# Optimization experiments

Measured on AMD Instinct MI355X. Metric: run time of the kernel, lower is better.

Reference implementation:

```python
import jax, jax.numpy as jnp
import numpy as np

STRIDES = (8, 16, 32)
NC = 80            # num_classes
BINS = 16          # dfl_bins
TOPK = 10          # tal_topk
TAL_ALPHA, TAL_BETA = 0.5, 6.0   # ultralytics TaskAlignedAssigner defaults
EPS = 1e-9
FOCAL_A, FOCAL_G = 0.25, 2.0
W_CLS, W_IOU, W_DFL = 0.5, 7.5, 1.5


def _make_grid(H, W, stride):
    ys, xs = jnp.meshgrid(jnp.arange(H, dtype=jnp.float32), jnp.arange(W, dtype=jnp.float32), indexing='ij')
    return jnp.stack([(xs + 0.5) * stride, (ys + 0.5) * stride], -1).reshape(H * W, 2)


def _flatten(p):
    # (B,C,H,W) -> cls (B,N,NC), dfl (B,N,4,BINS); channel layout = [4*BINS dfl | NC cls]
    B, C, H, W = p.shape
    p = p.transpose(0, 2, 3, 1).reshape(B, H * W, C)
    return p[..., 4 * BINS:], p[..., :4 * BINS].reshape(B, H * W, 4, BINS)


def _pairwise_iou(gt, pr):
    # gt (B,G,4), pr (B,N,4) -> iou (B,G,N)
    g = gt[:, :, None]
    p = pr[:, None]
    lt = jnp.maximum(g[..., :2], p[..., :2])
    rb = jnp.minimum(g[..., 2:], p[..., 2:])
    wh = jnp.clip(rb - lt, 0.0)
    inter = wh[..., 0] * wh[..., 1]
    ag = (g[..., 2] - g[..., 0]) * (g[..., 3] - g[..., 1])
    ap = jnp.clip(p[..., 2] - p[..., 0], 0.0) * jnp.clip(p[..., 3] - p[..., 1], 0.0)
    return inter / (ag + ap - inter + EPS)


def _ciou_loss(p, t):
    # elementwise CIoU loss, (...,4) xyxy -> (...)
    px1, py1, px2, py2 = p[..., 0], p[..., 1], p[..., 2], p[..., 3]
    tx1, ty1, tx2, ty2 = t[..., 0], t[..., 1], t[..., 2], t[..., 3]
    w1, h1 = px2 - px1, py2 - py1
    w2, h2 = tx2 - tx1, ty2 - ty1
    inter = jnp.clip(jnp.minimum(px2, tx2) - jnp.maximum(px1, tx1), 0.0) * \
            jnp.clip(jnp.minimum(py2, ty2) - jnp.maximum(py1, ty1), 0.0)
    union = w1 * h1 + w2 * h2 - inter + EPS
    iou = inter / union
    cw = jnp.maximum(px2, tx2) - jnp.minimum(px1, tx1)
    ch = jnp.maximum(py2, ty2) - jnp.minimum(py1, ty1)
    c2 = cw * cw + ch * ch + EPS
    rho2 = ((px1 + px2 - tx1 - tx2) ** 2 + (py1 + py2 - ty1 - ty2) ** 2) / 4.0
    v = (4.0 / np.pi ** 2) * (jnp.arctan(w2 / (h2 + EPS)) - jnp.arctan(w1 / (h1 + EPS))) ** 2
    alpha = jax.lax.stop_gradient(v / (v - iou + (1.0 + EPS)))
    return 1.0 - (iou - rho2 / c2 - v * alpha)


def _tal_assign(cls_prob, pred_boxes, grids, gt_bboxes, gt_labels):
    B, N, C = cls_prob.shape
    G = gt_bboxes.shape[1]
    idx = jnp.broadcast_to(gt_labels[:, None, :], (B, N, G))
    scores = jnp.take_along_axis(cls_prob, idx, axis=2).transpose(0, 2, 1)  # (B,G,N)
    overlaps = _pairwise_iou(gt_bboxes, pred_boxes)                          # (B,G,N)
    align = scores ** TAL_ALPHA * overlaps ** TAL_BETA
    x, y = grids[:, 0], grids[:, 1]
    in_gts = ((x[None, None] > gt_bboxes[..., 0:1]) & (x[None, None] < gt_bboxes[..., 2:3]) &
              (y[None, None] > gt_bboxes[..., 1:2]) & (y[None, None] < gt_bboxes[..., 3:4]))
    metric = jnp.where(in_gts, align, 0.0)
    vals, idxs = jax.lax.top_k(metric, TOPK)                                 # (B,G,TOPK)
    bi = jnp.arange(B)[:, None, None]
    gi = jnp.arange(G)[None, :, None]
    topk_mask = jnp.zeros((B, G, N), bool).at[bi, gi, idxs].set(vals > EPS)
    mask_pos = topk_mask & in_gts
    multi = mask_pos.sum(1) > 1                                              # (B,N)
    is_max = jnp.argmax(overlaps, 1)[:, None, :] == jnp.arange(G)[None, :, None]
    mask_pos = jnp.where(multi[:, None, :], is_max, mask_pos)
    fg = mask_pos.any(1)                                                     # (B,N)
    matched = jnp.argmax(mask_pos, 1)                                        # (B,N)
    mi = jnp.where(fg, matched, -1)
    b2 = jnp.arange(B)[:, None]
    tb = gt_bboxes[b2, matched]                                              # (B,N,4)
    tl = gt_labels[b2, matched]                                              # (B,N)
    mpf = mask_pos.astype(align.dtype)
    align_m = align * mpf
    ov_m = overlaps * mpf
    norm = (align_m * ov_m.max(-1, keepdims=True) / (align_m.max(-1, keepdims=True) + EPS)).max(1)
    ts = jax.nn.one_hot(tl, C, dtype=align.dtype) * norm[..., None] * fg[..., None]
    return ts, tb, fg, mi


def _dfl_targets(gt_bboxes, mi, fgf, grids, stride_map):
    # vectorized version of _make_dfl_targets: soft two-bin scatter per coord
    B, N = mi.shape
    b2 = jnp.arange(B)[:, None]
    boxes = gt_bboxes[b2, jnp.maximum(mi, 0)]                                # (B,N,4)
    cx, cy = grids[:, 0], grids[:, 1]
    d = jnp.stack([jnp.clip(cx - boxes[..., 0], 0.0), jnp.clip(cy - boxes[..., 1], 0.0),
                   jnp.clip(boxes[..., 2] - cx, 0.0), jnp.clip(boxes[..., 3] - cy, 0.0)], -1)
    d = jnp.clip(d / stride_map[None, :, None], 0.0, BINS - 1 - 1e-6)
    lo = jnp.floor(d)
    a = d - lo
    lo_i = lo.astype(jnp.int32)
    up_i = jnp.minimum(lo_i + 1, BINS - 1)
    td = jax.nn.one_hot(lo_i, BINS) * (1.0 - a)[..., None] + jax.nn.one_hot(up_i, BINS) * a[..., None]
    return td * fgf[..., None, None]                                         # (B,N,4,BINS)


def _focal_sum(logits, targets):
    logits = logits.reshape(-1, NC)
    targets = targets.reshape(-1, NC)
    p = jax.nn.sigmoid(logits)
    # stable BCE-with-logits
    ce = jnp.maximum(logits, 0.0) - logits * targets + jnp.log1p(jnp.exp(-jnp.abs(logits)))
    p_t = p * targets + (1.0 - p) * (1.0 - targets)
    a_t = targets * FOCAL_A + (1.0 - targets) * (1.0 - FOCAL_A)
    return (a_t * (1.0 - p_t) ** FOCAL_G * ce).sum()


def _loss(p0, p1, p2, gt_bboxes, gt_labels):
    cls_l, dfl_l, grid_l, str_l = [], [], [], []
    for p, s in zip((p0, p1, p2), STRIDES):
        c, d = _flatten(p)
        cls_l.append(c)
        dfl_l.append(d)
        H, W = p.shape[2], p.shape[3]
        grid_l.append(_make_grid(H, W, s))
        str_l.append(jnp.full((H * W,), float(s), jnp.float32))
    all_cls = jnp.concatenate(cls_l, 1)       # (B,N,NC)
    all_dfl = jnp.concatenate(dfl_l, 1)       # (B,N,4,BINS)
    grids = jnp.concatenate(grid_l, 0)        # (N,2)
    stride_map = jnp.concatenate(str_l, 0)    # (N,)
    # DFL decode: expectation over bins * stride -> ltrb -> xyxy
    dist = (jax.nn.softmax(all_dfl, -1) * jnp.arange(BINS, dtype=jnp.float32)).sum(-1) * stride_map[None, :, None]
    cx, cy = grids[:, 0], grids[:, 1]
    pred_boxes = jnp.stack([cx - dist[..., 0], cy - dist[..., 1], cx + dist[..., 2], cy + dist[..., 3]], -1)
    # assignment under stop_gradient (torch.no_grad in the original)
    cls_prob = jax.lax.stop_gradient(jax.nn.sigmoid(all_cls))
    pb_sg = jax.lax.stop_gradient(pred_boxes)
    ts, tb, fg, mi = _tal_assign(cls_prob, pb_sg, grids, gt_bboxes, gt_labels)
    ts = jax.lax.stop_gradient(ts)
    tb = jax.lax.stop_gradient(tb)
    fgf = fg.astype(jnp.float32)
    den = jnp.maximum(fg.sum(), 1).astype(jnp.float32)
    loss_iou = (_ciou_loss(pred_boxes, tb) * fgf).sum() / den
    tdfl = _dfl_targets(gt_bboxes, mi, fgf, grids, stride_map)
    loss_dfl = -(tdfl * jax.nn.log_softmax(all_dfl, -1)).sum() / den
    loss_cls = _focal_sum(all_cls, ts) / den
    return jnp.stack([W_IOU * loss_iou, W_DFL * loss_dfl, W_CLS * loss_cls])


def setup_inputs() -> dict:
    key = jax.random.key(0)
    ks = jax.random.split(key, 5)
    B, G = 16, 32
    p0 = jax.random.normal(ks[0], (B, 4 * BINS + NC, 80, 80), jnp.float32)
    p1 = jax.random.normal(ks[1], (B, 4 * BINS + NC, 40, 40), jnp.float32)
    p2 = jax.random.normal(ks[2], (B, 4 * BINS + NC, 20, 20), jnp.float32)
    u = jax.random.uniform(ks[3], (B, G, 4), jnp.float32)
    x1 = u[..., 0] * 560.0
    y1 = u[..., 1] * 560.0
    w = u[..., 2] * 140.0 + 20.0
    h = u[..., 3] * 140.0 + 20.0
    gt_bboxes = jnp.stack([x1, y1, jnp.minimum(x1 + w, 640.0), jnp.minimum(y1 + h, 640.0)], -1)
    gt_labels = jax.random.randint(ks[4], (B, G), 0, NC, jnp.int32)
    return {"p0": p0, "p1": p1, "p2": p2, "gt_bboxes": gt_bboxes, "gt_labels": gt_labels}


def reference(p0, p1, p2, gt_bboxes, gt_labels):
    return _loss(p0, p1, p2, gt_bboxes, gt_labels)
```

## Files before the change

kernel.cpp:

```cpp
#include <hip/hip_runtime.h>
#include <hip/hip_bf16.h>
#include <math.h>

#define NCC 80
#define BINS 16
#define NCH 144
#define NB 16
#define NG 32
#define NA 8400
#define HW0 6400
#define HW1 1600
#define HW2 400
#define TOPKK 10
#define EPSF 1e-9f
#define MAXC 832
#define MAXFG (NB*NG*TOPKK)
#define FGB2 20
#define NMASK (NB*NA)
#define DEC_BLOCKS 525
#define FOCAL_BLOCKS 2625
#define MAIN_BLOCKS (DEC_BLOCKS + FOCAL_BLOCKS)

__device__ __forceinline__ void anchor_geom(int n, float& cx, float& cy, float& st){
    if(n < HW0){ int y=n/80, x=n-y*80; st=8.f; cx=(x+0.5f)*8.f; cy=(y+0.5f)*8.f; }
    else if(n < HW0+HW1){ int m=n-HW0; int y=m/40, x=m-y*40; st=16.f; cx=(x+0.5f)*16.f; cy=(y+0.5f)*16.f; }
    else { int m=n-(HW0+HW1); int y=m/20, x=m-y*20; st=32.f; cx=(x+0.5f)*32.f; cy=(y+0.5f)*32.f; }
}

__device__ __forceinline__ const float* level_base(const float* p0, const float* p1, const float* p2,
                                                   int b, int n, int& m, int& hw){
    if(n < HW0){ m=n; hw=HW0; return p0 + (size_t)b*NCH*HW0; }
    if(n < HW0+HW1){ m=n-HW0; hw=HW1; return p1 + (size_t)b*NCH*HW1; }
    m=n-(HW0+HW1); hw=HW2; return p2 + (size_t)b*NCH*HW2;
}

__device__ __forceinline__ float iou_gp(float gx1,float gy1,float gx2,float gy2,
                                        float px1,float py1,float px2,float py2){
    float ltx = fmaxf(gx1, px1), lty = fmaxf(gy1, py1);
    float rbx = fminf(gx2, px2), rby = fminf(gy2, py2);
    float w = fmaxf(rbx-ltx, 0.f), h = fmaxf(rby-lty, 0.f);
    float inter = w*h;
    float ag = (gx2-gx1)*(gy2-gy1);
    float ap = fmaxf(px2-px1,0.f)*fmaxf(py2-py1,0.f);
    return inter/(ag+ap-inter+EPSF);
}

__device__ __forceinline__ float focal0(float x, float& p, float& ce0){
    float ax = fabsf(x);
    float e  = __expf(-ax);
    float r  = 1.f/(1.f+e);
    p   = (x >= 0.f) ? r : 1.f - r;
    ce0 = fmaxf(x,0.f) + __logf(1.f+e);
    return 0.75f*p*p*ce0;
}

__global__ __launch_bounds__(256) void k_main(const float* __restrict__ p0, const float* __restrict__ p1,
                                              const float* __restrict__ p2, float* __restrict__ boxc,
                                              float* __restrict__ lsev,
                                              unsigned* __restrict__ maskg, float* __restrict__ amax,
                                              float* __restrict__ omax, int* __restrict__ cnt,
                                              float* __restrict__ pcls){
    int tid = threadIdx.x;
    if(blockIdx.x < DEC_BLOCKS){
        int l = blockIdx.x*256 + tid;
        maskg[l] = 0u;
        if(l < NB*NG){ amax[l] = 0.f; omax[l] = 0.f; }
        if(l == 0) *cnt = 0;
        int q = l % 2100;
        int j = (l / 2100) & 3;
        int b = l / 8400;
        const float* pl; int hw, m, n0, D; float st;
        if(q < 1600){ pl=p0; hw=HW0; m=4*q;        n0=m;         D=80; st=8.f; }
        else if(q < 2000){ pl=p1; hw=HW1; m=4*(q-1600); n0=HW0+m;     D=40; st=16.f; }
        else { pl=p2; hw=HW2; m=4*(q-2000); n0=HW0+HW1+m; D=20; st=32.f; }
        const float* ch = pl + ((size_t)b*NCH + j*BINS)*hw + m;
        float4 v[BINS];
        float4 mx = make_float4(-1e30f,-1e30f,-1e30f,-1e30f);
        #pragma unroll
        for(int k=0;k<BINS;k++){
            v[k] = *(const float4*)(ch + (size_t)k*hw);
            mx.x=fmaxf(mx.x,v[k].x); mx.y=fmaxf(mx.y,v[k].y);
            mx.z=fmaxf(mx.z,v[k].z); mx.w=fmaxf(mx.w,v[k].w);
        }
        float4 s = make_float4(0,0,0,0), acc = make_float4(0,0,0,0);
        #pragma unroll
        for(int k=0;k<BINS;k++){
            float fk=(float)k; float e;
            e=__expf(v[k].x-mx.x); s.x+=e; acc.x+=e*fk;
            e=__expf(v[k].y-mx.y); s.y+=e; acc.y+=e*fk;
            e=__expf(v[k].z-mx.z); s.z+=e; acc.z+=e*fk;
            e=__expf(v[k].w-mx.w); s.w+=e; acc.w+=e*fk;
        }
        float4 lse = make_float4(mx.x+__logf(s.x), mx.y+__logf(s.y),
                                 mx.z+__logf(s.z), mx.w+__logf(s.w));
        *(float4*)(lsev + (size_t)j*NB*NA + (size_t)b*NA + n0) = lse;
        float4 d = make_float4(acc.x/s.x*st, acc.y/s.y*st, acc.z/s.z*st, acc.w/s.w*st);
        int row = m / D, col = m - row*D;
        float cy = (row+0.5f)*st;
        float cx0=(col+0.5f)*st, cx1=(col+1.5f)*st, cx2=(col+2.5f)*st, cx3=(col+3.5f)*st;
        float4 o;
        if(j==0)      o = make_float4(cx0-d.x, cx1-d.y, cx2-d.z, cx3-d.w);
        else if(j==1) o = make_float4(cy -d.x, cy -d.y, cy -d.z, cy -d.w);
        else if(j==2) o = make_float4(cx0+d.x, cx1+d.y, cx2+d.z, cx3+d.w);
        else          o = make_float4(cy +d.x, cy +d.y, cy +d.z, cy +d.w);
        *(float4*)(boxc + (size_t)j*NB*NA + (size_t)b*NA + n0) = o;
    } else {
        __shared__ float s4[4];
        int blk = blockIdx.x - DEC_BLOCKS;
        int t = blk*256 + tid;
        float acc = 0.f;
        #pragma unroll
        for(int it=0; it<4; ++it){
            int i4 = t + it*672000;
            const float4* src;
            if(i4 < 2048000){
                int b = i4 / 128000; int r = i4 - b*128000;
                src = (const float4*)(p0 + (size_t)b*921600 + 409600) + r;
            } else if(i4 < 2560000){
                int j = i4 - 2048000; int b = j / 32000; int r = j - b*32000;
                src = (const float4*)(p1 + (size_t)b*230400 + 102400) + r;
            } else {
                int j = i4 - 2560000; int b = j / 8000; int r = j - b*8000;
                src = (const float4*)(p2 + (size_t)b*57600 + 25600) + r;
            }
            float4 x4 = *src;
            float p, c;
            acc += focal0(x4.x, p, c);
            acc += focal0(x4.y, p, c);
            acc += focal0(x4.z, p, c);
            acc += focal0(x4.w, p, c);
        }
        #pragma unroll
        for(int off=32; off; off>>=1) acc += __shfl_down(acc, off);
        if((tid&63)==0) s4[tid>>6] = acc;
        __syncthreads();
        if(tid==0) pcls[blk] = s4[0]+s4[1]+s4[2]+s4[3];
    }
}

__global__ __launch_bounds__(256) void k_assign(const float* __restrict__ p0, const float* __restrict__ p1,
                                                const float* __restrict__ p2, const float* __restrict__ boxc,
                                                const float* __restrict__ gtb, const int* __restrict__ gtl,
                                                unsigned* __restrict__ maskg){
    __shared__ float metric[MAXC];
    __shared__ int   candn[MAXC];
    __shared__ float rv[4]; __shared__ int ri[4];
    __shared__ float sbest;
    int g = blockIdx.x, b = blockIdx.y, tid = threadIdx.x;
    const float* gb = gtb + ((size_t)b*NG + g)*4;
    float gx1=gb[0], gy1=gb[1], gx2=gb[2], gy2=gb[3];
    int label = gtl[b*NG+g];
    const float* bx1 = boxc + (size_t)b*NA;
    const float* by1 = bx1 + (size_t)NB*NA;
    const float* bx2 = by1 + (size_t)NB*NA;
    const float* by2 = bx2 + (size_t)NB*NA;

    int xs[3], ys[3], nxv[3], cc[3];
    #pragma unroll
    for(int lvl=0; lvl<3; lvl++){
        float s = (float)(8<<lvl); int D = 80>>lvl;
        int x0 = max(0, (int)floorf(gx1/s - 0.5f));
        int x1 = min(D-1, (int)ceilf (gx2/s - 0.5f));
        int y0 = max(0, (int)floorf(gy1/s - 0.5f));
        int y1 = min(D-1, (int)ceilf (gy2/s - 0.5f));
        xs[lvl]=x0; ys[lvl]=y0;
        nxv[lvl]=max(0, x1-x0+1);
        int nyv=max(0, y1-y0+1);
        cc[lvl]=nxv[lvl]*nyv;
    }
    int t0 = cc[0], t01 = cc[0]+cc[1], total = t01+cc[2];

    for(int c=tid; c<total; c+=256){
        int lvl, rel;
        if(c < t0){ lvl=0; rel=c; }
        else if(c < t01){ lvl=1; rel=c-t0; }
        else { lvl=2; rel=c-t01; }
        int yy = ys[lvl] + rel / nxv[lvl];
        int xx = xs[lvl] + rel % nxv[lvl];
        int D = 80>>lvl; float s = (float)(8<<lvl);
        int off = (lvl==0)?0:((lvl==1)?HW0:(HW0+HW1));
        int n = off + yy*D + xx;
        float cx = (xx+0.5f)*s, cy = (yy+0.5f)*s;
        float met = 0.f;
        if((cx>gx1)&&(cx<gx2)&&(cy>gy1)&&(cy<gy2)){
            float ov = iou_gp(gx1,gy1,gx2,gy2, bx1[n],by1[n],bx2[n],by2[n]);
            int m,hw; const float* base = level_base(p0,p1,p2,b,n,m,hw);
            float x = base[(size_t)(4*BINS+label)*hw + m];
            float sg = 1.f/(1.f+__expf(-x));
            float o2 = ov*ov;
            met = sqrtf(sg)*(o2*o2*o2);
        }
        metric[c] = met; candn[c] = n;
    }
    __syncthreads();

    for(int k=0;k<TOPKK;k++){
        float bv = -1.f; int bi = 0x7fffffff;
        for(int c=tid; c<total; c+=256){
            float v = metric[c];
            if(v > bv){ bv=v; bi=c; }
        }
        #pragma unroll
        for(int o=1; o<64; o<<=1){
            float ov = __shfl_xor(bv, o);
            int   oi = __shfl_xor(bi, o);
            if(ov > bv || (ov == bv && oi < bi)){ bv=ov; bi=oi; }
        }
        if((tid&63)==0){ rv[tid>>6]=bv; ri[tid>>6]=bi; }
        __syncthreads();
        if(tid==0){
            float fb=rv[0]; int fi=ri[0];
            #pragma unroll
            for(int w=1; w<4; w++)
                if(rv[w]>fb || (rv[w]==fb && ri[w]<fi)){ fb=rv[w]; fi=ri[w]; }
            sbest = fb;
            if(fb > EPSF){
                metric[fi] = -1.f;
                atomicOr(&maskg[(size_t)b*NA + candn[fi]], 1u<<g);
            }
        }
        __syncthreads();
        if(sbest <= EPSF) break;
    }
}

__global__ __launch_bounds__(256) void k_resolve(const float* __restrict__ p0, const float* __restrict__ p1,
                                                 const float* __restrict__ p2, const float* __restrict__ boxc,
                                                 const float* __restrict__ gtb, const int* __restrict__ gtl,
                                                 const unsigned* __restrict__ maskg,
                                                 float* __restrict__ amax, float* __restrict__ omax,
                                                 int* __restrict__ cnt, unsigned* __restrict__ fglist,
                                                 float* __restrict__ fgalign, float* __restrict__ fgx){
    __shared__ float sgt[NG*4];
    __shared__ int wcnt[4];
    __shared__ int sbase;
    int tid = threadIdx.x; int b = blockIdx.y;
    int wv = tid >> 6, lane = tid & 63;
    if(tid < NG*4) sgt[tid] = gtb[(size_t)b*NG*4 + tid];
    __syncthreads();
    int n = blockIdx.x*256 + tid;
    size_t bn = (size_t)b*NA + n;
    unsigned mask = (n < NA) ? maskg[bn] : 0u;
    bool fg = (mask != 0u);

    int match = 0; float ov = 0.f, av = 0.f, x = 0.f;
    if(fg){
        float px1 = boxc[bn], py1 = boxc[(size_t)NB*NA+bn],
              px2 = boxc[2*(size_t)NB*NA+bn], py2 = boxc[3*(size_t)NB*NA+bn];
        if(__popc(mask) > 1){
            float best = -1.f; int bi = 0;
            for(int g=0; g<NG; g++){
                float o = iou_gp(sgt[g*4],sgt[g*4+1],sgt[g*4+2],sgt[g*4+3],px1,py1,px2,py2);
                if(o > best){ best=o; bi=g; }
            }
            match = bi; ov = best;
        } else {
            match = __ffs(mask)-1;
            ov = iou_gp(sgt[match*4],sgt[match*4+1],sgt[match*4+2],sgt[match*4+3],px1,py1,px2,py2);
        }
        int label = gtl[b*NG+match];
        int m,hw; const float* base = level_base(p0,p1,p2,b,n,m,hw);
        x = base[(size_t)(4*BINS+label)*hw + m];
        float sg = 1.f/(1.f+__expf(-x));
        float ov2 = ov*ov;
        av = sqrtf(sg)*(ov2*ov2*ov2);
        atomicMax((int*)&amax[b*NG+match], __float_as_int(av));
        atomicMax((int*)&omax[b*NG+match], __float_as_int(ov));
    }
    unsigned long long bal = __ballot(fg);
    if(lane==0) wcnt[wv] = __popcll(bal);
    __syncthreads();
    if(tid==0){
        int tot = wcnt[0]+wcnt[1]+wcnt[2]+wcnt[3];
        sbase = tot ? atomicAdd(cnt, tot) : 0;
    }
    __syncthreads();
    if(fg){
        int woff = 0;
        for(int w=0; w<wv; w++) woff += wcnt[w];
        int before = __popcll(bal & ((1ull<<lane)-1ull));
        int pos = sbase + woff + before;
        fglist[pos]  = (unsigned)bn | ((unsigned)match << 18);
        fgalign[pos] = av;
        fgx[pos]     = x;
    }
}

__global__ __launch_bounds__(256) void k_fg(const float* __restrict__ p0, const float* __restrict__ p1,
                                            const float* __restrict__ p2, const float* __restrict__ boxc,
                                            const float* __restrict__ lsev, const float* __restrict__ gtb,
                                            const float* __restrict__ amax, const float* __restrict__ omax,
                                            const int* __restrict__ cnt, const unsigned* __restrict__ fglist,
                                            const float* __restrict__ fgalign, const float* __restrict__ fgx,
                                            float* __restrict__ piou, float* __restrict__ pdfl,
                                            float* __restrict__ pfix){
    __shared__ float siou[4], sdfl[4], sfix[4];
    int tid = threadIdx.x, wv = tid>>6, lane = tid&63;
    int i = blockIdx.x*256 + tid;
    float iou_l = 0.f, dfl_l = 0.f, fix_l = 0.f;
    if(i < *cnt){
        unsigned e = fglist[i];
        int bn = e & 0x3FFFF;
        int g  = e >> 18;
        int b  = bn / NA;
        int n  = bn - b*NA;
        float align = fgalign[i];
        float norm = align * omax[b*NG+g] / (amax[b*NG+g] + EPSF);
        const float* gb = gtb + ((size_t)b*NG+g)*4;
        float tx1=gb[0], ty1=gb[1], tx2=gb[2], ty2=gb[3];
        float px1 = boxc[bn], py1 = boxc[(size_t)NB*NA+bn],
              px2 = boxc[2*(size_t)NB*NA+bn], py2 = boxc[3*(size_t)NB*NA+bn];
        int m,hw; const float* base = level_base(p0,p1,p2,b,n,m,hw);
        float cx,cy,st; anchor_geom(n,cx,cy,st);
        float dt4[4] = { cx-tx1, cy-ty1, tx2-cx, ty2-cy };
        #pragma unroll
        for(int j=0;j<4;j++){
            float d = fminf(fmaxf(dt4[j],0.f)/st, 14.999999f);
            float lo = floorf(d); float a = d-lo;
            int li = (int)lo; int ui = min(li+1, BINS-1);
            float lse = lsev[(size_t)j*NB*NA + bn];
            float xlo = base[(size_t)(j*BINS+li)*hw + m];
            float xup = base[(size_t)(j*BINS+ui)*hw + m];
            dfl_l += -((1.f-a)*(xlo-lse) + a*(xup-lse));
        }
        float w1=px2-px1, h1=py2-py1, w2=tx2-tx1, h2=ty2-ty1;
        float inter = fmaxf(fminf(px2,tx2)-fmaxf(px1,tx1),0.f) *
                      fmaxf(fminf(py2,ty2)-fmaxf(py1,ty1),0.f);
        float uni = w1*h1 + w2*h2 - inter + EPSF;
        float iou = inter/uni;
        float cwd = fmaxf(px2,tx2)-fminf(px1,tx1);
        float chd = fmaxf(py2,ty2)-fminf(py1,ty1);
        float c2 = cwd*cwd + chd*chd + EPSF;
        float dx = px1+px2-tx1-tx2, dy = py1+py2-ty1-ty2;
        float rho2 = (dx*dx + dy*dy)*0.25f;
        float dv = atanf(w2/(h2+EPSF)) - atanf(w1/(h1+EPSF));
        float v = 0.40528473456935108577f*dv*dv;
        float alpha = v/(v - iou + 1.f + EPSF);
        iou_l = 1.f - (iou - rho2/c2 - v*alpha);
        float fx = fgx[i];
        float p, ce0;
        float f0 = focal0(fx, p, ce0);
        float tv = norm;
        float cet = ce0 - fx*tv;
        float pt = p*tv + (1.f-p)*(1.f-tv);
        float at = 0.25f*tv + 0.75f*(1.f-tv);
        float om = 1.f-pt;
        fix_l = at*om*om*cet - f0;
    }
    #pragma unroll
    for(int o=32; o; o>>=1){
        iou_l += __shfl_down(iou_l, o);
        dfl_l += __shfl_down(dfl_l, o);
        fix_l += __shfl_down(fix_l, o);
    }
    if(lane==0){ siou[wv]=iou_l; sdfl[wv]=dfl_l; sfix[wv]=fix_l; }
    __syncthreads();
    if(tid==0){
        piou[blockIdx.x] = siou[0]+siou[1]+siou[2]+siou[3];
        pdfl[blockIdx.x] = sdfl[0]+sdfl[1]+sdfl[2]+sdfl[3];
        pfix[blockIdx.x] = sfix[0]+sfix[1]+sfix[2]+sfix[3];
    }
}

__global__ __launch_bounds__(256) void k_final(const float* __restrict__ pcls, const float* __restrict__ piou,
                                               const float* __restrict__ pdfl, const float* __restrict__ pfix,
                                               const int* __restrict__ cnt, float* __restrict__ out){
    __shared__ float sa[4], sb[4], sc[4], sd[4];
    int tid = threadIdx.x, wv = tid>>6, lane = tid&63;
    float A = 0.f, B = 0.f, C = 0.f, D = 0.f;
    for(int t=tid; t<FOCAL_BLOCKS; t+=256) A += pcls[t];
    if(tid < FGB2){ B = piou[tid]; C = pdfl[tid]; D = pfix[tid]; }
    #pragma unroll
    for(int o=32; o; o>>=1){
        A += __shfl_down(A, o);
        B += __shfl_down(B, o);
        C += __shfl_down(C, o);
        D += __shfl_down(D, o);
    }
    if(lane==0){ sa[wv]=A; sb[wv]=B; sc[wv]=C; sd[wv]=D; }
    __syncthreads();
    if(tid==0){
        float a  = sa[0]+sa[1]+sa[2]+sa[3];
        float bb = sb[0]+sb[1]+sb[2]+sb[3];
        float cc = sc[0]+sc[1]+sc[2]+sc[3];
        float dd = sd[0]+sd[1]+sd[2]+sd[3];
        int c = *cnt;
        float den = (float)(c > 1 ? c : 1);
        out[0] = 7.5f * bb / den;
        out[1] = 1.5f * cc / den;
        out[2] = 0.5f * (a + dd) / den;
    }
}

extern "C" void kernel_launch(void* const* d_in, const int* in_sizes, int n_in,
                              void* d_out, int out_size, void* d_ws, size_t ws_size,
                              hipStream_t stream) {
    (void)in_sizes; (void)n_in; (void)out_size; (void)ws_size;
    const float* p0  = (const float*)d_in[0];
    const float* p1  = (const float*)d_in[1];
    const float* p2  = (const float*)d_in[2];
    const float* gtb = (const float*)d_in[3];
    const int*   gtl = (const int*)d_in[4];
    float* out = (float*)d_out;

    char* ws = (char*)d_ws;
    const size_t COMP = (size_t)NB*NA*4;
    size_t off = 0;
    int*      cnt    = (int*)     (ws + off); off += 16;
    float*    amax   = (float*)   (ws + off); off += NB*NG*4;
    float*    omax   = (float*)   (ws + off); off += NB*NG*4;
    unsigned* maskg  = (unsigned*)(ws + off); off += COMP;
    float*    boxc   = (float*)   (ws + off); off += 4*COMP;
    float*    lsev   = (float*)   (ws + off); off += 4*COMP;
    unsigned* fglist = (unsigned*)(ws + off); off += MAXFG*4;
    float*    fgalign= (float*)   (ws + off); off += MAXFG*4;
    float*    fgx    = (float*)   (ws + off); off += MAXFG*4;
    float*    pcls   = (float*)   (ws + off); off += FOCAL_BLOCKS*4;
    float*    piou   = (float*)   (ws + off); off += FGB2*4;
    float*    pdfl   = (float*)   (ws + off); off += FGB2*4;
    float*    pfix   = (float*)   (ws + off); off += FGB2*4;

    dim3 blk(256);
    k_main   <<<MAIN_BLOCKS,   blk, 0, stream>>>(p0,p1,p2, boxc, lsev, maskg, amax, omax, cnt, pcls);
    k_assign <<<dim3(NG,NB),   blk, 0, stream>>>(p0,p1,p2, boxc, gtb, gtl, maskg);
    k_resolve<<<dim3(33,NB),   blk, 0, stream>>>(p0,p1,p2, boxc, gtb, gtl, maskg,
                                                 amax, omax, cnt, fglist, fgalign, fgx);
    k_fg     <<<FGB2,          blk, 0, stream>>>(p0,p1,p2, boxc, lsev, gtb, amax, omax,
                                                 cnt, fglist, fgalign, fgx, piou, pdfl, pfix);
    k_final  <<<1,             blk, 0, stream>>>(pcls, piou, pdfl, pfix, cnt, out);
}
```

Before: 144.6 us.

## Fuse foreground CIoU/DFL loss into resolve kernel and focal fix into final

Removes the separate k_fg launch. The CIoU and DFL terms, which need no global normalization, are now computed directly in k_resolve, with per-block partial sums written out. The focal correction depends on the global amax/omax, so it moves into the single-block k_final, which loops over all foreground entries. This saves one kernel launch and the compacted-list round trip, at the cost of serializing the focal-fix work (up to about 5k entries) in one block and adding divergent work in the resolve blocks.

```diff
diff --git a/kernel.cpp b/kernel.cpp
--- a/kernel.cpp
+++ b/kernel.cpp
@@ -15,8 +15,8 @@
 #define EPSF 1e-9f
 #define MAXC 832
 #define MAXFG (NB*NG*TOPKK)
-#define FGB2 20
 #define NMASK (NB*NA)
+#define NRES 528
 #define DEC_BLOCKS 525
 #define FOCAL_BLOCKS 2625
 #define MAIN_BLOCKS (DEC_BLOCKS + FOCAL_BLOCKS)
@@ -226,14 +226,17 @@
 
 __global__ __launch_bounds__(256) void k_resolve(const float* __restrict__ p0, const float* __restrict__ p1,
                                                  const float* __restrict__ p2, const float* __restrict__ boxc,
+                                                 const float* __restrict__ lsev,
                                                  const float* __restrict__ gtb, const int* __restrict__ gtl,
                                                  const unsigned* __restrict__ maskg,
                                                  float* __restrict__ amax, float* __restrict__ omax,
-                                                 int* __restrict__ cnt, unsigned* __restrict__ fglist,
-                                                 float* __restrict__ fgalign, float* __restrict__ fgx){
+                                                 int* __restrict__ cnt, int* __restrict__ fgbg,
+                                                 float* __restrict__ fgalign, float* __restrict__ fgx,
+                                                 float* __restrict__ piou, float* __restrict__ pdfl){
     __shared__ float sgt[NG*4];
     __shared__ int wcnt[4];
     __shared__ int sbase;
+    __shared__ float siou[4], sdfl[4];
     int tid = threadIdx.x; int b = blockIdx.y;
     int wv = tid >> 6, lane = tid & 63;
     if(tid < NG*4) sgt[tid] = gtb[(size_t)b*NG*4 + tid];
@@ -243,10 +246,12 @@
     unsigned mask = (n < NA) ? maskg[bn] : 0u;
     bool fg = (mask != 0u);
 
-    int match = 0; float ov = 0.f, av = 0.f, x = 0.f;
+    int match = 0; float av = 0.f, x = 0.f;
+    float iou_l = 0.f, dfl_l = 0.f;
     if(fg){
         float px1 = boxc[bn], py1 = boxc[(size_t)NB*NA+bn],
               px2 = boxc[2*(size_t)NB*NA+bn], py2 = boxc[3*(size_t)NB*NA+bn];
+        float ov;
         if(__popc(mask) > 1){
             float best = -1.f; int bi = 0;
             for(int g=0; g<NG; g++){
@@ -266,51 +271,21 @@
         av = sqrtf(sg)*(ov2*ov2*ov2);
         atomicMax((int*)&amax[b*NG+match], __float_as_int(av));
         atomicMax((int*)&omax[b*NG+match], __float_as_int(ov));
-    }
-    unsigned long long bal = __ballot(fg);
-    if(lane==0) wcnt[wv] = __popcll(bal);
-    __syncthreads();
-    if(tid==0){
-        int tot = wcnt[0]+wcnt[1]+wcnt[2]+wcnt[3];
-        sbase = tot ? atomicAdd(cnt, tot) : 0;
-    }
-    __syncthreads();
-    if(fg){
-        int woff = 0;
-        for(int w=0; w<wv; w++) woff += wcnt[w];
-        int before = __popcll(bal & ((1ull<<lane)-1ull));
-        int pos = sbase + woff + before;
-        fglist[pos]  = (unsigned)bn | ((unsigned)match << 18);
-        fgalign[pos] = av;
-        fgx[pos]     = x;
-    }
-}
-
-__global__ __launch_bounds__(256) void k_fg(const float* __restrict__ p0, const float* __restrict__ p1,
-                                            const float* __restrict__ p2, const float* __restrict__ boxc,
-                                            const float* __restrict__ lsev, const float* __restrict__ gtb,
-                                            const float* __restrict__ amax, const float* __restrict__ omax,
-                                            const int* __restrict__ cnt, const unsigned* __restrict__ fglist,
-                                            const float* __restrict__ fgalign, const float* __restrict__ fgx,
-                                            float* __restrict__ piou, float* __restrict__ pdfl,
-                                            float* __restrict__ pfix){
-    __shared__ float siou[4], sdfl[4], sfix[4];
-    int tid = threadIdx.x, wv = tid>>6, lane = tid&63;
-    int i = blockIdx.x*256 + tid;
-    float iou_l = 0.f, dfl_l = 0.f, fix_l = 0.f;
-    if(i < *cnt){
-        unsigned e = fglist[i];
-        int bn = e & 0x3FFFF;
-        int g  = e >> 18;
-        int b  = bn / NA;
-        int n  = bn - b*NA;
-        float align = fgalign[i];
-        float norm = align * omax[b*NG+g] / (amax[b*NG+g] + EPSF);
-        const float* gb = gtb + ((size_t)b*NG+g)*4;
-        float tx1=gb[0], ty1=gb[1], tx2=gb[2], ty2=gb[3];
-        float px1 = boxc[bn], py1 = boxc[(size_t)NB*NA+bn],
-              px2 = boxc[2*(size_t)NB*NA+bn], py2 = boxc[3*(size_t)NB*NA+bn];
-        int m,hw; const float* base = level_base(p0,p1,p2,b,n,m,hw);
+        float tx1=sgt[match*4], ty1=sgt[match*4+1], tx2=sgt[match*4+2], ty2=sgt[match*4+3];
+        float w1=px2-px1, h1=py2-py1, w2=tx2-tx1, h2=ty2-ty1;
+        float inter = fmaxf(fminf(px2,tx2)-fmaxf(px1,tx1),0.f) *
+                      fmaxf(fminf(py2,ty2)-fmaxf(py1,ty1),0.f);
+        float uni = w1*h1 + w2*h2 - inter + EPSF;
+        float iou = inter/uni;
+        float cwd = fmaxf(px2,tx2)-fminf(px1,tx1);
+        float chd = fmaxf(py2,ty2)-fminf(py1,ty1);
+        float c2 = cwd*cwd + chd*chd + EPSF;
+        float ddx = px1+px2-tx1-tx2, ddy = py1+py2-ty1-ty2;
+        float rho2 = (ddx*ddx + ddy*ddy)*0.25f;
+        float dv = atanf(w2/(h2+EPSF)) - atanf(w1/(h1+EPSF));
+        float v = 0.40528473456935108577f*dv*dv;
+        float alpha = v/(v - iou + 1.f + EPSF);
+        iou_l = 1.f - (iou - rho2/c2 - v*alpha);
         float cx,cy,st; anchor_geom(n,cx,cy,st);
         float dt4[4] = { cx-tx1, cy-ty1, tx2-cx, ty2-cy };
         #pragma unroll
@@ -323,53 +298,65 @@
             float xup = base[(size_t)(j*BINS+ui)*hw + m];
             dfl_l += -((1.f-a)*(xlo-lse) + a*(xup-lse));
         }
-        float w1=px2-px1, h1=py2-py1, w2=tx2-tx1, h2=ty2-ty1;
-        float inter = fmaxf(fminf(px2,tx2)-fmaxf(px1,tx1),0.f) *
-                      fmaxf(fminf(py2,ty2)-fmaxf(py1,ty1),0.f);
-        float uni = w1*h1 + w2*h2 - inter + EPSF;
-        float iou = inter/uni;
-        float cwd = fmaxf(px2,tx2)-fminf(px1,tx1);
-        float chd = fmaxf(py2,ty2)-fminf(py1,ty1);
-        float c2 = cwd*cwd + chd*chd + EPSF;
-        float dx = px1+px2-tx1-tx2, dy = py1+py2-ty1-ty2;
-        float rho2 = (dx*dx + dy*dy)*0.25f;
-        float dv = atanf(w2/(h2+EPSF)) - atanf(w1/(h1+EPSF));
-        float v = 0.40528473456935108577f*dv*dv;
-        float alpha = v/(v - iou + 1.f + EPSF);
-        iou_l = 1.f - (iou - rho2/c2 - v*alpha);
-        float fx = fgx[i];
-        float p, ce0;
-        float f0 = focal0(fx, p, ce0);
-        float tv = norm;
-        float cet = ce0 - fx*tv;
-        float pt = p*tv + (1.f-p)*(1.f-tv);
-        float at = 0.25f*tv + 0.75f*(1.f-tv);
-        float om = 1.f-pt;
-        fix_l = at*om*om*cet - f0;
+    }
+    unsigned long long bal = __ballot(fg);
+    if(lane==0) wcnt[wv] = __popcll(bal);
+    __syncthreads();
+    if(tid==0){
+        int tot = wcnt[0]+wcnt[1]+wcnt[2]+wcnt[3];
+        sbase = tot ? atomicAdd(cnt, tot) : 0;
+    }
+    __syncthreads();
+    if(fg){
+        int woff = 0;
+        for(int w=0; w<wv; w++) woff += wcnt[w];
+        int before = __popcll(bal & ((1ull<<lane)-1ull));
+        int pos = sbase + woff + before;
+        fgbg[pos]    = b*NG + match;
+        fgalign[pos] = av;
+        fgx[pos]     = x;
     }
     #pragma unroll
     for(int o=32; o; o>>=1){
         iou_l += __shfl_down(iou_l, o);
         dfl_l += __shfl_down(dfl_l, o);
-        fix_l += __shfl_down(fix_l, o);
-    }
-    if(lane==0){ siou[wv]=iou_l; sdfl[wv]=dfl_l; sfix[wv]=fix_l; }
+    }
+    if(lane==0){ siou[wv]=iou_l; sdfl[wv]=dfl_l; }
     __syncthreads();
     if(tid==0){
-        piou[blockIdx.x] = siou[0]+siou[1]+siou[2]+siou[3];
-        pdfl[blockIdx.x] = sdfl[0]+sdfl[1]+sdfl[2]+sdfl[3];
-        pfix[blockIdx.x] = sfix[0]+sfix[1]+sfix[2]+sfix[3];
+        int blk = blockIdx.y*33 + blockIdx.x;
+        piou[blk] = siou[0]+siou[1]+siou[2]+siou[3];
+        pdfl[blk] = sdfl[0]+sdfl[1]+sdfl[2]+sdfl[3];
     }
 }
 
 __global__ __launch_bounds__(256) void k_final(const float* __restrict__ pcls, const float* __restrict__ piou,
-                                               const float* __restrict__ pdfl, const float* __restrict__ pfix,
+                                               const float* __restrict__ pdfl,
+                                               const float* __restrict__ amax, const float* __restrict__ omax,
+                                               const int* __restrict__ fgbg, const float* __restrict__ fgalign,
+                                               const float* __restrict__ fgx,
                                                const int* __restrict__ cnt, float* __restrict__ out){
+    __shared__ float sam[NB*NG], som[NB*NG];
     __shared__ float sa[4], sb[4], sc[4], sd[4];
     int tid = threadIdx.x, wv = tid>>6, lane = tid&63;
+    for(int t=tid; t<NB*NG; t+=256){ sam[t]=amax[t]; som[t]=omax[t]; }
+    __syncthreads();
+    int c = *cnt;
     float A = 0.f, B = 0.f, C = 0.f, D = 0.f;
     for(int t=tid; t<FOCAL_BLOCKS; t+=256) A += pcls[t];
-    if(tid < FGB2){ B = piou[tid]; C = pdfl[tid]; D = pfix[tid]; }
+    for(int t=tid; t<NRES; t+=256){ B += piou[t]; C += pdfl[t]; }
+    for(int i=tid; i<c; i+=256){
+        int bg = fgbg[i];
+        float norm = fgalign[i] * som[bg] / (sam[bg] + EPSF);
+        float fx = fgx[i];
+        float p, ce0;
+        float f0 = focal0(fx, p, ce0);
+        float cet = ce0 - fx*norm;
+        float pt = p*norm + (1.f-p)*(1.f-norm);
+        float at = 0.25f*norm + 0.75f*(1.f-norm);
+        float om = 1.f-pt;
+        D += at*om*om*cet - f0;
+    }
     #pragma unroll
     for(int o=32; o; o>>=1){
         A += __shfl_down(A, o);
@@ -384,7 +371,6 @@
         float bb = sb[0]+sb[1]+sb[2]+sb[3];
         float cc = sc[0]+sc[1]+sc[2]+sc[3];
         float dd = sd[0]+sd[1]+sd[2]+sd[3];
-        int c = *cnt;
         float den = (float)(c > 1 ? c : 1);
         out[0] = 7.5f * bb / den;
         out[1] = 1.5f * cc / den;
@@ -412,20 +398,18 @@
     unsigned* maskg  = (unsigned*)(ws + off); off += COMP;
     float*    boxc   = (float*)   (ws + off); off += 4*COMP;
     float*    lsev   = (float*)   (ws + off); off += 4*COMP;
-    unsigned* fglist = (unsigned*)(ws + off); off += MAXFG*4;
+    int*      fgbg   = (int*)     (ws + off); off += MAXFG*4;
     float*    fgalign= (float*)   (ws + off); off += MAXFG*4;
     float*    fgx    = (float*)   (ws + off); off += MAXFG*4;
     float*    pcls   = (float*)   (ws + off); off += FOCAL_BLOCKS*4;
-    float*    piou   = (float*)   (ws + off); off += FGB2*4;
-    float*    pdfl   = (float*)   (ws + off); off += FGB2*4;
-    float*    pfix   = (float*)   (ws + off); off += FGB2*4;
+    float*    piou   = (float*)   (ws + off); off += NRES*4;
+    float*    pdfl   = (float*)   (ws + off); off += NRES*4;
 
     dim3 blk(256);
     k_main   <<<MAIN_BLOCKS,   blk, 0, stream>>>(p0,p1,p2, boxc, lsev, maskg, amax, omax, cnt, pcls);
     k_assign <<<dim3(NG,NB),   blk, 0, stream>>>(p0,p1,p2, boxc, gtb, gtl, maskg);
-    k_resolve<<<dim3(33,NB),   blk, 0, stream>>>(p0,p1,p2, boxc, gtb, gtl, maskg,
-                                                 amax, omax, cnt, fglist, fgalign, fgx);
-    k_fg     <<<FGB2,          blk, 0, stream>>>(p0,p1,p2, boxc, lsev, gtb, amax, omax,
-                                                 cnt, fglist, fgalign, fgx, piou, pdfl, pfix);
-    k_final  <<<1,             blk, 0, stream>>>(pcls, piou, pdfl, pfix, cnt, out);
-}
+    k_resolve<<<dim3(33,NB),   blk, 0, stream>>>(p0,p1,p2, boxc, lsev, gtb, gtl, maskg,
+                                                 amax, omax, cnt, fgbg, fgalign, fgx, piou, pdfl);
+    k_final  <<<1,             blk, 0, stream>>>(pcls, piou, pdfl, amax, omax,
+                                                 fgbg, fgalign, fgx, cnt, out);
+}
```

Measured after the change: 148.8 us. +2.9%, slower.
